# Kernel tuning notes

Hardware: AMD Instinct MI355X
Metric: run time of the kernel (lower is better)

## Reference

```python
import jax, jax.numpy as jnp
import numpy as np

# Model dims (match init_kwargs)
NUM_EXPERTS = 8
TOP_K = 2
D_MODEL = 1024
D_FF = 4096
BATCH = 4
SEQ = 2048


def setup_inputs() -> dict:
    key = jax.random.key(0)
    ks = jax.random.split(key, 6)
    x = jax.random.normal(ks[0], (BATCH, SEQ, D_MODEL), dtype=jnp.float32)
    # Linear gating network: logits = x @ Wg + bg
    Wg = jax.random.normal(ks[1], (D_MODEL, NUM_EXPERTS), dtype=jnp.float32) * (D_MODEL ** -0.5)
    bg = jnp.zeros((NUM_EXPERTS,), dtype=jnp.float32)
    # Per-expert 2-layer FFN params, stacked over expert axis E
    W1 = jax.random.normal(ks[2], (NUM_EXPERTS, D_MODEL, D_FF), dtype=jnp.float32) * (D_MODEL ** -0.5)
    b1 = jnp.zeros((NUM_EXPERTS, D_FF), dtype=jnp.float32)
    W2 = jax.random.normal(ks[3], (NUM_EXPERTS, D_FF, D_MODEL), dtype=jnp.float32) * (D_FF ** -0.5)
    b2 = jnp.zeros((NUM_EXPERTS, D_MODEL), dtype=jnp.float32)
    return {"x": x, "Wg": Wg, "bg": bg, "W1": W1, "b1": b1, "W2": W2, "b2": b2}


def reference(x, Wg, bg, W1, b1, W2, b2):
    B, S, D = x.shape
    E = Wg.shape[1]
    xf = x.reshape(-1, D)  # [T, D], T = B*S tokens

    # --- Linear gating: softmax probs, top-k hard assignment mask ---
    gate_logits = xf @ Wg + bg                      # [T, E]
    gate_probs = jax.nn.softmax(gate_logits, -1)    # [T, E]
    _, top_idx = jax.lax.top_k(gate_probs, TOP_K)   # [T, K]
    # expert_assignment = sum over k of one_hot(indices) -> {0,1} mask [T, E]
    assign = jnp.sum(jax.nn.one_hot(top_idx, E, dtype=gate_probs.dtype), axis=-2)

    # --- All experts process all tokens (faithful to _process_hard_routing) ---
    # h: [E, T, F]; out_e: [E, T, D]
    h = jax.nn.gelu(jnp.einsum('td,edf->etf', xf, W1) + b1[:, None, :])
    out_e = jnp.einsum('etf,efd->etd', h, W2) + b2[:, None, :]

    # --- Weighted combine: expert_output * gate_prob * top-k mask, sum over E ---
    w = (gate_probs * assign).T[:, :, None]         # [E, T, 1]
    out = jnp.sum(out_e * w, axis=0)                # [T, D]
    return out.reshape(B, S, D)
```

## Files before the change

### kernel.cpp

```cpp
#include <hip/hip_runtime.h>
#include <hip/hip_bf16.h>
#include <stdint.h>

#define T_TOK 8192
#define DM 1024
#define DF 4096
#define NE 8
#define NSLOT 136

typedef __attribute__((ext_vector_type(8))) short short8;
typedef __attribute__((ext_vector_type(8))) unsigned short ushort8;
typedef __attribute__((ext_vector_type(4))) float f32x4;

#define AS1 __attribute__((address_space(1)))
#define AS3 __attribute__((address_space(3)))

#define NB_GATE (T_TOK / 4)
#define NB_T1 ((DF / 64) * (DM / 64) * NE)
#define NB_T2 ((DM / 64) * (DF / 64) * NE)

static __device__ __forceinline__ unsigned short f2bf(float f) {
  union { float f; unsigned int u; } c; c.f = f;
  unsigned int u = c.u;
  unsigned int r = (u + 0x7FFFu + ((u >> 16) & 1u)) >> 16;
  return (unsigned short)r;
}

static __device__ __forceinline__ float gelu_tanh(float v) {
  float y = 0.7978845608028654f * (v + 0.044715f * v * v * v);
  float ay = fabsf(y);
  float e = __expf(-2.0f * ay);
  float th = (1.0f - e) / (1.0f + e);
  th = copysignf(th, y);
  return 0.5f * v * (1.0f + th);
}

__global__ void k_probe(float* out, float v, int n) {
  int i = blockIdx.x * blockDim.x + threadIdx.x;
  for (; i < n; i += gridDim.x * blockDim.x) out[i] = v;
}

__global__ void k_prep(const float* __restrict__ x, unsigned short* __restrict__ xb,
                       const float* __restrict__ Wg, const float* __restrict__ bg,
                       const float* __restrict__ W1, unsigned short* __restrict__ w1t,
                       const float* __restrict__ W2, unsigned short* __restrict__ w2t,
                       const float* __restrict__ b2, float* __restrict__ out,
                       int* __restrict__ choice2, float* __restrict__ wts) {
  __shared__ float tile[64][65];
  int bid = blockIdx.x;

  if (bid < NB_GATE) {
    int wave = threadIdx.x >> 6, lane = threadIdx.x & 63;
    int t = bid * 4 + wave;
    const float* xr = x + (size_t)t * DM;
    unsigned short* xo = xb + (size_t)t * DM;
    double acc[NE];
#pragma unroll
    for (int e = 0; e < NE; ++e) acc[e] = 0.0;
#pragma unroll
    for (int i = 0; i < 4; ++i) {
      int d = lane * 4 + i * 256;
      float4 v = *(const float4*)(xr + d);
      ushort4 o;
      o.x = f2bf(v.x); o.y = f2bf(v.y); o.z = f2bf(v.z); o.w = f2bf(v.w);
      *(ushort4*)(xo + d) = o;
      float xv[4] = {v.x, v.y, v.z, v.w};
#pragma unroll
      for (int q = 0; q < 4; ++q) {
        const float4* wg = (const float4*)(Wg + (size_t)(d + q) * NE);
        float4 w0 = wg[0], w1 = wg[1];
        acc[0] += (double)xv[q] * w0.x; acc[1] += (double)xv[q] * w0.y;
        acc[2] += (double)xv[q] * w0.z; acc[3] += (double)xv[q] * w0.w;
        acc[4] += (double)xv[q] * w1.x; acc[5] += (double)xv[q] * w1.y;
        acc[6] += (double)xv[q] * w1.z; acc[7] += (double)xv[q] * w1.w;
      }
    }
#pragma unroll
    for (int off = 32; off; off >>= 1)
#pragma unroll
      for (int e = 0; e < NE; ++e) acc[e] += __shfl_xor(acc[e], off);
    int e1i = 0, e2i = 0;
    float w1v = 0.f, w2v = 0.f;
    if (lane == 0) {
      float lg[NE];
#pragma unroll
      for (int e = 0; e < NE; ++e) lg[e] = (float)acc[e] + bg[e];
      float m = lg[0];
#pragma unroll
      for (int e = 1; e < NE; ++e) m = fmaxf(m, lg[e]);
      float s = 0.f, p[NE];
#pragma unroll
      for (int e = 0; e < NE; ++e) { p[e] = expf(lg[e] - m); s += p[e]; }
      float inv = 1.f / s;
      int i1 = 0;
#pragma unroll
      for (int e = 1; e < NE; ++e) if (lg[e] > lg[i1]) i1 = e;
      int i2 = (i1 == 0) ? 1 : 0;
#pragma unroll
      for (int e = 0; e < NE; ++e) if (e != i1 && lg[e] > lg[i2]) i2 = e;
      e1i = i1; e2i = i2;
      w1v = p[i1] * inv; w2v = p[i2] * inv;
      choice2[2 * t] = i1;     wts[2 * t] = w1v;
      choice2[2 * t + 1] = i2; wts[2 * t + 1] = w2v;
    }
    e1i = __shfl(e1i, 0); e2i = __shfl(e2i, 0);
    w1v = __shfl(w1v, 0); w2v = __shfl(w2v, 0);
#pragma unroll
    for (int i = 0; i < 4; ++i) {
      int d = lane * 4 + i * 256;
      float4 a = *(const float4*)(b2 + (size_t)e1i * DM + d);
      float4 b = *(const float4*)(b2 + (size_t)e2i * DM + d);
      float4 o;
      o.x = w1v * a.x + w2v * b.x; o.y = w1v * a.y + w2v * b.y;
      o.z = w1v * a.z + w2v * b.z; o.w = w1v * a.w + w2v * b.w;
      *(float4*)(out + (size_t)t * DM + d) = o;
    }
    return;
  }

  const float* src;
  unsigned short* dst;
  int R, C, r0, c0;
  if (bid < NB_GATE + NB_T1) {
    int b2i = bid - NB_GATE;
    int e = b2i >> 10, rem = b2i & 1023;
    int byy = rem >> 6, bxx = rem & 63;
    R = DM; C = DF; r0 = byy * 64; c0 = bxx * 64;
    src = W1 + (size_t)e * DM * DF;
    dst = w1t + (size_t)e * DM * DF;
  } else {
    int b2i = bid - NB_GATE - NB_T1;
    int e = b2i >> 10, rem = b2i & 1023;
    int byy = rem >> 4, bxx = rem & 15;
    R = DF; C = DM; r0 = byy * 64; c0 = bxx * 64;
    src = W2 + (size_t)e * DF * DM;
    dst = w2t + (size_t)e * DF * DM;
  }
  int tx = threadIdx.x & 15, ty = threadIdx.x >> 4;
#pragma unroll
  for (int i = 0; i < 4; ++i) {
    int r = ty + i * 16;
    float4 v = *(const float4*)(src + (size_t)(r0 + r) * C + c0 + tx * 4);
    tile[r][tx * 4 + 0] = v.x; tile[r][tx * 4 + 1] = v.y;
    tile[r][tx * 4 + 2] = v.z; tile[r][tx * 4 + 3] = v.w;
  }
  __syncthreads();
  int tx2 = threadIdx.x & 7, ty2 = threadIdx.x >> 3;
#pragma unroll
  for (int i = 0; i < 2; ++i) {
    int c = ty2 + i * 32;
    ushort8 o;
#pragma unroll
    for (int j = 0; j < 8; ++j) o[j] = f2bf(tile[tx2 * 8 + j][c]);
    *(ushort8*)(dst + (size_t)(c0 + c) * R + r0 + tx2 * 8) = o;
  }
}

__global__ void k_bucket(const int* __restrict__ choice2, const float* __restrict__ wts,
                         int* __restrict__ counts, int* __restrict__ offsets,
                         int* __restrict__ btok, float* __restrict__ bw,
                         int* __restrict__ work) {
  __shared__ int c2[16];
  int tid = threadIdx.x;
  int w = tid >> 6, lane = tid & 63;
  int e = w & 7, h = w >> 3;
  int base0 = h * T_TOK;
  unsigned long long below = (lane == 0) ? 0ull : ((1ull << lane) - 1ull);
  int cnt = 0;
  for (int i0 = 0; i0 < T_TOK; i0 += 64) {
    int ce = choice2[base0 + i0 + lane];
    cnt += (int)__popcll(__ballot(ce == e));
  }
  if (lane == 0) c2[w] = cnt;
  __syncthreads();
  if (tid == 0) {
    int s = 0;
    for (int q = 0; q < NE; ++q) {
      counts[q] = c2[q] + c2[q + 8];
      offsets[q] = s; s += counts[q];
    }
    int idx = 0;
    for (int q = 0; q < NE; ++q) {
      int nby = (counts[q] + 127) >> 7;
      for (int j = 0; j < nby; ++j) work[idx++] = (q << 20) | (j << 7);
    }
    while (idx < NSLOT) work[idx++] = -1;
  }
  __syncthreads();
  int pos = h ? c2[e] : 0;
  for (int i0 = 0; i0 < T_TOK; i0 += 64) {
    int idx = base0 + i0 + lane;
    int ce = choice2[idx];
    float wt = wts[idx];
    unsigned long long m = __ballot(ce == e);
    if (ce == e) {
      int r = (int)__popcll(m & below);
      btok[e * T_TOK + pos + r] = idx >> 1;
      bw[e * T_TOK + pos + r] = wt;
    }
    pos += (int)__popcll(m);
  }
}


__global__ __launch_bounds__(256, 4) void k_gemm1(
    const unsigned short* __restrict__ xb,
    const unsigned short* __restrict__ w1t,
    const float* __restrict__ b1,
    const int* __restrict__ counts, const int* __restrict__ offsets,
    const int* __restrict__ btok, const int* __restrict__ work,
    unsigned short* __restrict__ H,
    int gx) {
  __shared__ __align__(16) unsigned short ldsA[128 * 64];
  __shared__ __align__(16) unsigned short ldsB[128 * 64];
  __shared__ int toksh[128];

  int nwg = gx * NSLOT;
  int bid = blockIdx.x;
  int wg = (bid & 7) * (nwg >> 3) + (bid >> 3);
  int slot = wg / gx;
  int bx = wg - slot * gx;
  int pk = work[slot];
  if (pk < 0) return;
  int e = pk >> 20;
  int m0 = pk & 0xFFFFF;
  int cnt = counts[e];
  int eoff = offsets[e];
  int f0 = bx * 128;
  int tid = threadIdx.x;
  int wave = tid >> 6, lane = tid & 63;

  for (int i = tid; i < 128; i += 256) {
    int p = m0 + i; if (p >= cnt) p = cnt - 1;
    toksh[i] = btok[e * T_TOK + p];
  }
  __syncthreads();

  int slin = lane & 7, rsub = lane >> 3;
  int ksl8 = (slin ^ rsub) * 8;

  const unsigned short* srcA[4];
  const unsigned short* srcB[4];
  int ldsg[4];
#pragma unroll
  for (int j = 0; j < 4; ++j) {
    int g = j * 4 + wave;
    int m = g * 8 + rsub;
    srcA[j] = xb + (size_t)toksh[m] * DM + ksl8;
    srcB[j] = w1t + ((size_t)e * DF + f0 + m) * DM + ksl8;
    ldsg[j] = g * 512;
  }

  auto stage = [&](int ks) {
#pragma unroll
    for (int j = 0; j < 4; ++j) {
      __builtin_amdgcn_global_load_lds((const AS1 void*)(srcA[j] + (size_t)ks * 64),
                                       (AS3 void*)(&ldsA[ldsg[j]]), 16, 0, 0);
      __builtin_amdgcn_global_load_lds((const AS1 void*)(srcB[j] + (size_t)ks * 64),
                                       (AS3 void*)(&ldsB[ldsg[j]]), 16, 0, 0);
    }
  };

  int wm = wave >> 1, wn = wave & 1;
  int lrow = lane & 15, khi = lane >> 4;
  f32x4 acc[4][4];
#pragma unroll
  for (int m = 0; m < 4; ++m)
#pragma unroll
    for (int n = 0; n < 4; ++n) acc[m][n] = (f32x4){0.f, 0.f, 0.f, 0.f};

  auto compute = [&]() {
#pragma unroll
    for (int kk = 0; kk < 2; ++kk) {
      int kslot = kk * 4 + khi;
      short8 af[4], bfv[4];
#pragma unroll
      for (int m = 0; m < 4; ++m) {
        int row = wm * 64 + m * 16 + lrow;
        int slotx = kslot ^ (row & 7);
        af[m] = *(const short8*)(&ldsA[row * 64 + slotx * 8]);
      }
#pragma unroll
      for (int n = 0; n < 4; ++n) {
        int row = wn * 64 + n * 16 + lrow;
        int slotx = kslot ^ (row & 7);
        bfv[n] = *(const short8*)(&ldsB[row * 64 + slotx * 8]);
      }
#pragma unroll
      for (int m = 0; m < 4; ++m)
#pragma unroll
        for (int n = 0; n < 4; ++n)
          acc[m][n] = __builtin_amdgcn_mfma_f32_16x16x32_bf16(af[m], bfv[n], acc[m][n], 0, 0, 0);
    }
  };

  const int nk = DM / 64;
  for (int ks = 0; ks < nk; ++ks) {
    stage(ks);
    __syncthreads();
    compute();
    __syncthreads();
  }

#pragma unroll
  for (int m = 0; m < 4; ++m) {
    int rbase = wm * 64 + m * 16 + khi * 4;
#pragma unroll
    for (int j = 0; j < 4; ++j) {
      int pos = m0 + rbase + j;
      if (pos < cnt) {
        size_t hrow = (size_t)(eoff + pos) * DF;
#pragma unroll
        for (int n = 0; n < 4; ++n) {
          int fl = f0 + wn * 64 + n * 16 + lrow;
          float v = acc[m][n][j] + b1[e * DF + fl];
          H[hrow + fl] = f2bf(gelu_tanh(v));
        }
      }
    }
  }
}

__global__ __launch_bounds__(256, 4) void k_gemm2(
    const unsigned short* __restrict__ H,
    const unsigned short* __restrict__ w2t,
    const int* __restrict__ counts, const int* __restrict__ offsets,
    const int* __restrict__ btok, const float* __restrict__ bw,
    const int* __restrict__ work,
    float* __restrict__ out, int gx) {
  __shared__ __align__(16) unsigned short ldsA[128 * 64];
  __shared__ __align__(16) unsigned short ldsB[128 * 64];
  __shared__ int toksh[128];
  __shared__ float wsh[128];

  int nwg = gx * NSLOT;
  int bid = blockIdx.x;
  int wg = (bid & 7) * (nwg >> 3) + (bid >> 3);
  int slot = wg / gx;
  int bx = wg - slot * gx;
  int pk = work[slot];
  if (pk < 0) return;
  int e = pk >> 20;
  int m0 = pk & 0xFFFFF;
  int cnt = counts[e];
  int eoff = offsets[e];
  int d0 = bx * 128;
  int tid = threadIdx.x;
  int wave = tid >> 6, lane = tid & 63;

  for (int i = tid; i < 128; i += 256) {
    int p = m0 + i; if (p >= cnt) p = cnt - 1;
    toksh[i] = btok[e * T_TOK + p];
    wsh[i] = bw[e * T_TOK + p];
  }
  __syncthreads();

  int slin = lane & 7, rsub = lane >> 3;
  int ksl8 = (slin ^ rsub) * 8;

  const unsigned short* srcA[4];
  const unsigned short* srcB[4];
  int ldsg[4];
#pragma unroll
  for (int j = 0; j < 4; ++j) {
    int g = j * 4 + wave;
    int m = g * 8 + rsub;
    int p = m0 + m; if (p >= cnt) p = cnt - 1;
    srcA[j] = H + (size_t)(eoff + p) * DF + ksl8;
    srcB[j] = w2t + ((size_t)e * DM + d0 + m) * DF + ksl8;
    ldsg[j] = g * 512;
  }

  auto stage = [&](int ks) {
#pragma unroll
    for (int j = 0; j < 4; ++j) {
      __builtin_amdgcn_global_load_lds((const AS1 void*)(srcA[j] + (size_t)ks * 64),
                                       (AS3 void*)(&ldsA[ldsg[j]]), 16, 0, 0);
      __builtin_amdgcn_global_load_lds((const AS1 void*)(srcB[j] + (size_t)ks * 64),
                                       (AS3 void*)(&ldsB[ldsg[j]]), 16, 0, 0);
    }
  };

  int wm = wave >> 1, wn = wave & 1;
  int lrow = lane & 15, khi = lane >> 4;
  f32x4 acc[4][4];
#pragma unroll
  for (int m = 0; m < 4; ++m)
#pragma unroll
    for (int n = 0; n < 4; ++n) acc[m][n] = (f32x4){0.f, 0.f, 0.f, 0.f};

  auto compute = [&]() {
#pragma unroll
    for (int kk = 0; kk < 2; ++kk) {
      int kslot = kk * 4 + khi;
      short8 af[4], bfv[4];
#pragma unroll
      for (int m = 0; m < 4; ++m) {
        int row = wm * 64 + m * 16 + lrow;
        int slotx = kslot ^ (row & 7);
        af[m] = *(const short8*)(&ldsA[row * 64 + slotx * 8]);
      }
#pragma unroll
      for (int n = 0; n < 4; ++n) {
        int row = wn * 64 + n * 16 + lrow;
        int slotx = kslot ^ (row & 7);
        bfv[n] = *(const short8*)(&ldsB[row * 64 + slotx * 8]);
      }
#pragma unroll
      for (int m = 0; m < 4; ++m)
#pragma unroll
        for (int n = 0; n < 4; ++n)
          acc[m][n] = __builtin_amdgcn_mfma_f32_16x16x32_bf16(af[m], bfv[n], acc[m][n], 0, 0, 0);
    }
  };

  const int nk = DF / 64;
  for (int ks = 0; ks < nk; ++ks) {
    stage(ks);
    __syncthreads();
    compute();
    __syncthreads();
  }

#pragma unroll
  for (int m = 0; m < 4; ++m) {
    int rbase = wm * 64 + m * 16 + khi * 4;
#pragma unroll
    for (int j = 0; j < 4; ++j) {
      int lr = rbase + j;
      int pos = m0 + lr;
      if (pos < cnt) {
        int tok = toksh[lr];
        float wgt = wsh[lr];
#pragma unroll
        for (int n = 0; n < 4; ++n) {
          int dc = d0 + wn * 64 + n * 16 + lrow;
          atomicAdd(&out[(size_t)tok * DM + dc], wgt * acc[m][n][j]);
        }
      }
    }
  }
}

extern "C" void kernel_launch(void* const* d_in, const int* in_sizes, int n_in,
                              void* d_out, int out_size, void* d_ws, size_t ws_size,
                              hipStream_t stream) {
  const float* x  = (const float*)d_in[0];
  const float* Wg = (const float*)d_in[1];
  const float* bg = (const float*)d_in[2];
  const float* W1 = (const float*)d_in[3];
  const float* b1 = (const float*)d_in[4];
  const float* W2 = (const float*)d_in[5];
  const float* b2 = (const float*)d_in[6];
  float* out = (float*)d_out;

  uint8_t* ws = (uint8_t*)d_ws;
  size_t off = 0;
  auto alloc = [&](size_t bytes) {
    size_t o = off;
    off = (off + bytes + 255) & ~(size_t)255;
    return o;
  };
  size_t o_counts = alloc(NE * 4);
  size_t o_offsets = alloc(NE * 4);
  size_t o_work = alloc(NSLOT * 4);
  size_t o_choice = alloc((size_t)2 * T_TOK * 4);
  size_t o_wts = alloc((size_t)2 * T_TOK * 4);
  size_t o_btok = alloc((size_t)NE * T_TOK * 4);
  size_t o_bw = alloc((size_t)NE * T_TOK * 4);
  size_t o_xb = alloc((size_t)T_TOK * DM * 2);
  size_t o_w1t = alloc((size_t)NE * DF * DM * 2);
  size_t o_w2t = alloc((size_t)NE * DM * DF * 2);
  size_t o_h = alloc((size_t)2 * T_TOK * DF * 2);

  if (off > ws_size) {
    k_probe<<<dim3(1024), dim3(256), 0, stream>>>(out, (float)(double)ws_size, out_size);
    return;
  }

  int* counts = (int*)(ws + o_counts);
  int* offsets = (int*)(ws + o_offsets);
  int* work = (int*)(ws + o_work);
  int* choice2 = (int*)(ws + o_choice);
  float* wtsp = (float*)(ws + o_wts);
  int* btok = (int*)(ws + o_btok);
  float* bwp = (float*)(ws + o_bw);
  unsigned short* xb = (unsigned short*)(ws + o_xb);
  unsigned short* w1t = (unsigned short*)(ws + o_w1t);
  unsigned short* w2t = (unsigned short*)(ws + o_w2t);
  unsigned short* Hbuf = (unsigned short*)(ws + o_h);

  k_prep<<<dim3(NB_GATE + NB_T1 + NB_T2), dim3(256), 0, stream>>>(
      x, xb, Wg, bg, W1, w1t, W2, w2t, b2, out, choice2, wtsp);
  k_bucket<<<dim3(1), dim3(1024), 0, stream>>>(choice2, wtsp, counts, offsets, btok, bwp, work);

  int g1x = DF / 128;
  int g2x = DM / 128;
  k_gemm1<<<dim3(g1x * NSLOT), dim3(256), 0, stream>>>(
      xb, w1t, b1, counts, offsets, btok, work, Hbuf, g1x);
  k_gemm2<<<dim3(g2x * NSLOT), dim3(256), 0, stream>>>(
      Hbuf, w2t, counts, offsets, btok, bwp, work, out, g2x);
}
```

Measured before the change: 578.5 us.

## Use 512-thread workgroups with 8 waves per 128x128 tile in both GEMMs

Both grouped GEMM kernels move from 4 waves to 8 waves per workgroup. Each wave now computes a 64x32 sub-tile instead of 64x64, which halves the accumulator registers per thread, and the staging loads are spread across twice as many threads. The goal is more waves in flight to hide global and LDS latency. The cost is more barrier participants and fewer MFMAs per wave for each LDS fragment read, so B-fragment reuse drops.

```diff
diff --git a/kernel.cpp b/kernel.cpp
--- a/kernel.cpp
+++ b/kernel.cpp
@@ -203,7 +203,7 @@
 }
 
 
-__global__ __launch_bounds__(256, 4) void k_gemm1(
+__global__ __launch_bounds__(512, 6) void k_gemm1(
     const unsigned short* __restrict__ xb,
     const unsigned short* __restrict__ w1t,
     const float* __restrict__ b1,
@@ -230,30 +230,27 @@
   int tid = threadIdx.x;
   int wave = tid >> 6, lane = tid & 63;
 
-  for (int i = tid; i < 128; i += 256) {
-    int p = m0 + i; if (p >= cnt) p = cnt - 1;
-    toksh[i] = btok[e * T_TOK + p];
+  if (tid < 128) {
+    int p = m0 + tid; if (p >= cnt) p = cnt - 1;
+    toksh[tid] = btok[e * T_TOK + p];
   }
   __syncthreads();
 
-  int slin = lane & 7, rsub = lane >> 3;
-  int ksl8 = (slin ^ rsub) * 8;
-
-  const unsigned short* srcA[4];
-  const unsigned short* srcB[4];
-  int ldsg[4];
-#pragma unroll
-  for (int j = 0; j < 4; ++j) {
-    int g = j * 4 + wave;
-    int m = g * 8 + rsub;
-    srcA[j] = xb + (size_t)toksh[m] * DM + ksl8;
-    srcB[j] = w1t + ((size_t)e * DF + f0 + m) * DM + ksl8;
-    ldsg[j] = g * 512;
+  const unsigned short* srcA[2];
+  const unsigned short* srcB[2];
+  int ldsg[2];
+#pragma unroll
+  for (int j = 0; j < 2; ++j) {
+    int s = j * 512 + tid;
+    int row = s >> 3, q = s & 7;
+    srcA[j] = xb + (size_t)toksh[row] * DM + ((q ^ (row & 7)) * 8);
+    srcB[j] = w1t + ((size_t)e * DF + f0 + row) * DM + ((q ^ (row & 7)) * 8);
+    ldsg[j] = s * 8;
   }
 
   auto stage = [&](int ks) {
 #pragma unroll
-    for (int j = 0; j < 4; ++j) {
+    for (int j = 0; j < 2; ++j) {
       __builtin_amdgcn_global_load_lds((const AS1 void*)(srcA[j] + (size_t)ks * 64),
                                        (AS3 void*)(&ldsA[ldsg[j]]), 16, 0, 0);
       __builtin_amdgcn_global_load_lds((const AS1 void*)(srcB[j] + (size_t)ks * 64),
@@ -261,19 +258,19 @@
     }
   };
 
-  int wm = wave >> 1, wn = wave & 1;
+  int wm = wave >> 2, wn = wave & 3;
   int lrow = lane & 15, khi = lane >> 4;
-  f32x4 acc[4][4];
+  f32x4 acc[4][2];
 #pragma unroll
   for (int m = 0; m < 4; ++m)
 #pragma unroll
-    for (int n = 0; n < 4; ++n) acc[m][n] = (f32x4){0.f, 0.f, 0.f, 0.f};
+    for (int n = 0; n < 2; ++n) acc[m][n] = (f32x4){0.f, 0.f, 0.f, 0.f};
 
   auto compute = [&]() {
 #pragma unroll
     for (int kk = 0; kk < 2; ++kk) {
       int kslot = kk * 4 + khi;
-      short8 af[4], bfv[4];
+      short8 af[4], bfv[2];
 #pragma unroll
       for (int m = 0; m < 4; ++m) {
         int row = wm * 64 + m * 16 + lrow;
@@ -281,15 +278,15 @@
         af[m] = *(const short8*)(&ldsA[row * 64 + slotx * 8]);
       }
 #pragma unroll
-      for (int n = 0; n < 4; ++n) {
-        int row = wn * 64 + n * 16 + lrow;
+      for (int n = 0; n < 2; ++n) {
+        int row = wn * 32 + n * 16 + lrow;
         int slotx = kslot ^ (row & 7);
         bfv[n] = *(const short8*)(&ldsB[row * 64 + slotx * 8]);
       }
 #pragma unroll
       for (int m = 0; m < 4; ++m)
 #pragma unroll
-        for (int n = 0; n < 4; ++n)
+        for (int n = 0; n < 2; ++n)
           acc[m][n] = __builtin_amdgcn_mfma_f32_16x16x32_bf16(af[m], bfv[n], acc[m][n], 0, 0, 0);
     }
   };
@@ -311,8 +308,8 @@
       if (pos < cnt) {
         size_t hrow = (size_t)(eoff + pos) * DF;
 #pragma unroll
-        for (int n = 0; n < 4; ++n) {
-          int fl = f0 + wn * 64 + n * 16 + lrow;
+        for (int n = 0; n < 2; ++n) {
+          int fl = f0 + wn * 32 + n * 16 + lrow;
           float v = acc[m][n][j] + b1[e * DF + fl];
           H[hrow + fl] = f2bf(gelu_tanh(v));
         }
@@ -321,7 +318,7 @@
   }
 }
 
-__global__ __launch_bounds__(256, 4) void k_gemm2(
+__global__ __launch_bounds__(512, 6) void k_gemm2(
     const unsigned short* __restrict__ H,
     const unsigned short* __restrict__ w2t,
     const int* __restrict__ counts, const int* __restrict__ offsets,
@@ -348,32 +345,29 @@
   int tid = threadIdx.x;
   int wave = tid >> 6, lane = tid & 63;
 
-  for (int i = tid; i < 128; i += 256) {
-    int p = m0 + i; if (p >= cnt) p = cnt - 1;
-    toksh[i] = btok[e * T_TOK + p];
-    wsh[i] = bw[e * T_TOK + p];
+  if (tid < 128) {
+    int p = m0 + tid; if (p >= cnt) p = cnt - 1;
+    toksh[tid] = btok[e * T_TOK + p];
+    wsh[tid] = bw[e * T_TOK + p];
   }
   __syncthreads();
 
-  int slin = lane & 7, rsub = lane >> 3;
-  int ksl8 = (slin ^ rsub) * 8;
-
-  const unsigned short* srcA[4];
-  const unsigned short* srcB[4];
-  int ldsg[4];
-#pragma unroll
-  for (int j = 0; j < 4; ++j) {
-    int g = j * 4 + wave;
-    int m = g * 8 + rsub;
-    int p = m0 + m; if (p >= cnt) p = cnt - 1;
-    srcA[j] = H + (size_t)(eoff + p) * DF + ksl8;
-    srcB[j] = w2t + ((size_t)e * DM + d0 + m) * DF + ksl8;
-    ldsg[j] = g * 512;
+  const unsigned short* srcA[2];
+  const unsigned short* srcB[2];
+  int ldsg[2];
+#pragma unroll
+  for (int j = 0; j < 2; ++j) {
+    int s = j * 512 + tid;
+    int row = s >> 3, q = s & 7;
+    int p = m0 + row; if (p >= cnt) p = cnt - 1;
+    srcA[j] = H + (size_t)(eoff + p) * DF + ((q ^ (row & 7)) * 8);
+    srcB[j] = w2t + ((size_t)e * DM + d0 + row) * DF + ((q ^ (row & 7)) * 8);
+    ldsg[j] = s * 8;
   }
 
   auto stage = [&](int ks) {
 #pragma unroll
-    for (int j = 0; j < 4; ++j) {
+    for (int j = 0; j < 2; ++j) {
       __builtin_amdgcn_global_load_lds((const AS1 void*)(srcA[j] + (size_t)ks * 64),
                                        (AS3 void*)(&ldsA[ldsg[j]]), 16, 0, 0);
       __builtin_amdgcn_global_load_lds((const AS1 void*)(srcB[j] + (size_t)ks * 64),
@@ -381,19 +375,19 @@
     }
   };
 
-  int wm = wave >> 1, wn = wave & 1;
+  int wm = wave >> 2, wn = wave & 3;
   int lrow = lane & 15, khi = lane >> 4;
-  f32x4 acc[4][4];
+  f32x4 acc[4][2];
 #pragma unroll
   for (int m = 0; m < 4; ++m)
 #pragma unroll
-    for (int n = 0; n < 4; ++n) acc[m][n] = (f32x4){0.f, 0.f, 0.f, 0.f};
+    for (int n = 0; n < 2; ++n) acc[m][n] = (f32x4){0.f, 0.f, 0.f, 0.f};
 
   auto compute = [&]() {
 #pragma unroll
     for (int kk = 0; kk < 2; ++kk) {
       int kslot = kk * 4 + khi;
-      short8 af[4], bfv[4];
+      short8 af[4], bfv[2];
 #pragma unroll
       for (int m = 0; m < 4; ++m) {
         int row = wm * 64 + m * 16 + lrow;
@@ -401,15 +395,15 @@
         af[m] = *(const short8*)(&ldsA[row * 64 + slotx * 8]);
       }
 #pragma unroll
-      for (int n = 0; n < 4; ++n) {
-        int row = wn * 64 + n * 16 + lrow;
+      for (int n = 0; n < 2; ++n) {
+        int row = wn * 32 + n * 16 + lrow;
         int slotx = kslot ^ (row & 7);
         bfv[n] = *(const short8*)(&ldsB[row * 64 + slotx * 8]);
       }
 #pragma unroll
       for (int m = 0; m < 4; ++m)
 #pragma unroll
-        for (int n = 0; n < 4; ++n)
+        for (int n = 0; n < 2; ++n)
           acc[m][n] = __builtin_amdgcn_mfma_f32_16x16x32_bf16(af[m], bfv[n], acc[m][n], 0, 0, 0);
     }
   };
@@ -433,8 +427,8 @@
         int tok = toksh[lr];
         float wgt = wsh[lr];
 #pragma unroll
-        for (int n = 0; n < 4; ++n) {
-          int dc = d0 + wn * 64 + n * 16 + lrow;
+        for (int n = 0; n < 2; ++n) {
+          int dc = d0 + wn * 32 + n * 16 + lrow;
           atomicAdd(&out[(size_t)tok * DM + dc], wgt * acc[m][n][j]);
         }
       }
@@ -496,8 +490,8 @@
 
   int g1x = DF / 128;
   int g2x = DM / 128;
-  k_gemm1<<<dim3(g1x * NSLOT), dim3(256), 0, stream>>>(
+  k_gemm1<<<dim3(g1x * NSLOT), dim3(512), 0, stream>>>(
       xb, w1t, b1, counts, offsets, btok, work, Hbuf, g1x);
-  k_gemm2<<<dim3(g2x * NSLOT), dim3(256), 0, stream>>>(
+  k_gemm2<<<dim3(g2x * NSLOT), dim3(512), 0, stream>>>(
       Hbuf, w2t, counts, offsets, btok, bwp, work, out, g2x);
 }
```

Result: slower. 836.2 us (+44.6%).
